# Kernel optimization log

Measured on AMD Instinct MI355X. Metric: run time of the kernel, lower is better.

## Reference

```python
import jax, jax.numpy as jnp
import numpy as np
import math

B, S, H, D = 8, 2048, 1024, 64  # batch, seq_len, hidden_dim, head_size

def setup_inputs() -> dict:
    key = jax.random.key(0)
    ks = jax.random.split(key, 7)
    lim = 1.0 / math.sqrt(H)  # torch Linear default init bound
    return {
        "x":  jax.random.normal(ks[0], (B, S, H), dtype=jnp.float32),
        "Wq": jax.random.uniform(ks[1], (H, D), jnp.float32, -lim, lim),
        "bq": jax.random.uniform(ks[2], (D,),   jnp.float32, -lim, lim),
        "Wk": jax.random.uniform(ks[3], (H, D), jnp.float32, -lim, lim),
        "bk": jax.random.uniform(ks[4], (D,),   jnp.float32, -lim, lim),
        "Wv": jax.random.uniform(ks[5], (H, D), jnp.float32, -lim, lim),
        "bv": jax.random.uniform(ks[6], (D,),   jnp.float32, -lim, lim),
    }

def reference(x, Wq, bq, Wk, bk, Wv, bv):
    # x: [B, S, H]
    q = x @ Wq + bq          # [B, S, D]
    k = x @ Wk + bk          # [B, S, D]
    v = x @ Wv + bv          # [B, S, D]
    scores = jnp.einsum("bsd,btd->bst", q, k)       # [B, S, S]
    causal = jnp.tril(jnp.ones((S, S), dtype=bool))
    scores = jnp.where(causal, scores, -jnp.inf)
    # NOTE: original module (faithfully) applies softmax FIRST, then divides
    # by sqrt(hidden_dim) -- it does NOT scale logits before softmax.
    weight = jax.nn.softmax(scores, axis=-1) / jnp.sqrt(jnp.float32(x.shape[-1]))
    # dropout p=0.0 -> identity
    return jnp.einsum("bst,btd->bsd", weight, v)     # [B, S, D]
```

## Files before the change

kernel.cpp:

```cpp
#include <hip/hip_runtime.h>


typedef float     f32x4 __attribute__((ext_vector_type(4)));
typedef _Float16  f16x8 __attribute__((ext_vector_type(8)));
typedef _Float16  f16x4 __attribute__((ext_vector_type(4)));

#define L2E 1.44269504088896340736f

__global__ __launch_bounds__(256) void wt_prep(const float* __restrict__ Wq,
                                               const float* __restrict__ Wk,
                                               const float* __restrict__ Wv,
                                               _Float16* __restrict__ WtF) {
  const int w  = blockIdx.x >> 4;
  const int kt = blockIdx.x & 15;
  const float* src = (w == 0) ? Wq : (w == 1 ? Wk : Wv);
  __shared__ _Float16 ls[64][72];
  const int t = threadIdx.x;
  {
    int rr = t >> 4;
    int c4 = (t & 15) * 4;
    #pragma unroll
    for (int ri = 0; ri < 4; ++ri) {
      int k = rr + ri * 16;
      f32x4 f = *(const f32x4*)&src[(size_t)(kt * 64 + k) * 64 + c4];
      #pragma unroll
      for (int j = 0; j < 4; ++j) ls[k][c4 + j] = (_Float16)f[j];
    }
  }
  __syncthreads();
  const int lane = t & 63, l16 = lane & 15, quad = lane >> 4;
  #pragma unroll
  for (int h = 0; h < 2; ++h) {
    int fid     = h * 4 + (t >> 6);
    int kstep_l = fid >> 2;
    int ntl     = fid & 3;
    int nt      = w * 4 + ntl;
    int kstep   = kt * 2 + kstep_l;
    f16x8 o;
    #pragma unroll
    for (int j = 0; j < 8; ++j) o[j] = ls[kstep_l * 32 + quad * 8 + j][ntl * 16 + l16];
    *(f16x8*)&WtF[((size_t)(kstep * 12 + nt) * 64 + lane) * 8] = o;
  }
}

__global__ __launch_bounds__(768) void qkv_gemm(const float* __restrict__ x,
                                                const _Float16* __restrict__ WtF,
                                                const float* __restrict__ bq,
                                                const float* __restrict__ bk,
                                                const float* __restrict__ bv,
                                                _Float16* __restrict__ qo,
                                                _Float16* __restrict__ ko,
                                                _Float16* __restrict__ vt) {
  __shared__ _Float16 xs[32 * 1024];
  const int tid  = threadIdx.x;
  const int wave = tid >> 6, lane = tid & 63;
  const int l16  = lane & 15, quad = lane >> 4;
  const int mhalf = wave / 6;
  const int ngrp  = wave - mhalf * 6;
  const int m0    = blockIdx.x * 32;

  if (tid < 512) {
    int row   = tid >> 4;
    int cbase = (tid & 15) * 4;
    const float* xrow = x + (size_t)(m0 + row) * 1024;
    int key = row & 7;
    #pragma unroll
    for (int j = 0; j < 16; ++j) {
      int col = cbase + j * 64;
      f32x4 f = *(const f32x4*)&xrow[col];
      f16x4 hh;
      #pragma unroll
      for (int e = 0; e < 4; ++e) hh[e] = (_Float16)f[e];
      int g   = col >> 3;
      int sub = col & 7;
      *(f16x4*)&xs[(size_t)row * 1024 + (size_t)((g ^ key) << 3) + sub] = hh;
    }
  }
  __syncthreads();

  f32x4 acc0 = (f32x4){0.f,0.f,0.f,0.f};
  f32x4 acc1 = (f32x4){0.f,0.f,0.f,0.f};
  const int arow = mhalf * 16 + l16;
  const _Float16* abase = xs + (size_t)arow * 1024;
  const int akey = arow & 7;
  const _Float16* wbase = WtF + ((size_t)(ngrp * 2) * 64 + lane) * 8;

  #pragma unroll 4
  for (int kstep = 0; kstep < 32; ++kstep) {
    f16x8 a = *(const f16x8*)(abase + (((kstep * 4 + quad) ^ akey) << 3));
    const _Float16* wk = wbase + (size_t)kstep * (12 * 64 * 8);
    f16x8 b0 = *(const f16x8*)(wk);
    f16x8 b1 = *(const f16x8*)(wk + 512);
    acc0 = __builtin_amdgcn_mfma_f32_16x16x32_f16(a, b0, acc0, 0, 0, 0);
    acc1 = __builtin_amdgcn_mfma_f32_16x16x32_f16(a, b1, acc1, 0, 0, 0);
  }

  f32x4 accs[2] = {acc0, acc1};
  #pragma unroll
  for (int i = 0; i < 2; ++i) {
    int nt  = ngrp * 2 + i;
    int col = nt * 16 + l16;
    float bias = (nt < 4) ? bq[col] : (nt < 8) ? bk[col - 64] : bv[col - 128];
    #pragma unroll
    for (int r = 0; r < 4; ++r) {
      int m = m0 + mhalf * 16 + quad * 4 + r;
      _Float16 hv = (_Float16)(accs[i][r] + bias);
      if (nt < 4)      qo[(size_t)m * 64 + col] = hv;
      else if (nt < 8) ko[(size_t)m * 64 + (col - 64)] = hv;
      else {
        int b = m >> 11, s = m & 2047;
        vt[((size_t)b * 64 + (col - 128)) * 2048 + s] = hv;
      }
    }
  }
}

__global__ __launch_bounds__(256) void attn(const _Float16* __restrict__ q,
                                            const _Float16* __restrict__ k,
                                            const _Float16* __restrict__ vt,
                                            _Float16* __restrict__ po,
                                            float* __restrict__ pm,
                                            float* __restrict__ pl) {
  const int bid = 575 - blockIdx.x;
  const int b   = blockIdx.y;
  int g = 0;
  #pragma unroll
  for (int gg = 0; gg < 7; ++gg) if (bid >= 8 * (gg + 1) * (gg + 2)) g = gg + 1;
  const int r   = bid - 8 * g * (g + 1);
  const int qi  = r / (g + 1);
  const int qt  = 16 * g + qi;
  const int s   = r - qi * (g + 1);
  const int q0  = qt * 16, kvend = q0 + 16;

  const int tid  = threadIdx.x;
  const int wave = tid >> 6, lane = tid & 63;
  const int l16  = lane & 15, quad = lane >> 4;
  const int kv0  = s * 256 + wave * 64;

  __shared__ float ow[4][64][17];
  __shared__ float mw[4][16], lw[4][16];
  _Float16* Plw = (_Float16*)&ow[wave][0][0];

  float m = -1e30f, l = 0.f;
  f32x4 o[4];
  #pragma unroll
  for (int i = 0; i < 4; ++i) o[i] = (f32x4){0.f, 0.f, 0.f, 0.f};

  if (kv0 < kvend) {
    const _Float16* qb = q  + (size_t)b * 2048 * 64;
    const _Float16* kb = k  + (size_t)b * 2048 * 64;
    const _Float16* vb = vt + (size_t)b * 64 * 2048;
    f16x8 qf0 = *(const f16x8*)&qb[(q0 + l16) * 64 + quad * 8];
    f16x8 qf1 = *(const f16x8*)&qb[(q0 + l16) * 64 + 32 + quad * 8];

    f32x4 sc[4];
    #pragma unroll
    for (int t = 0; t < 4; ++t) {
      int kvc = kv0 + t * 16;
      if (kvc < kvend) {
        f16x8 kf0 = *(const f16x8*)&kb[(kvc + l16) * 64 + quad * 8];
        f16x8 kf1 = *(const f16x8*)&kb[(kvc + l16) * 64 + 32 + quad * 8];
        f32x4 c = (f32x4){0.f, 0.f, 0.f, 0.f};
        c = __builtin_amdgcn_mfma_f32_16x16x32_f16(kf0, qf0, c, 0, 0, 0);
        c = __builtin_amdgcn_mfma_f32_16x16x32_f16(kf1, qf1, c, 0, 0, 0);
        sc[t] = c;
      } else sc[t] = (f32x4){-1e30f, -1e30f, -1e30f, -1e30f};
    }
    if (kv0 + 63 > q0) {
      #pragma unroll
      for (int t = 0; t < 4; ++t) {
        #pragma unroll
        for (int rr = 0; rr < 4; ++rr) {
          int skv = kv0 + t * 16 + quad * 4 + rr;
          if (skv > q0 + l16) sc[t][rr] = -1e30f;
        }
      }
    }
    float mx = sc[0][0];
    #pragma unroll
    for (int t = 0; t < 4; ++t)
      #pragma unroll
      for (int rr = 0; rr < 4; ++rr) mx = fmaxf(mx, sc[t][rr]);
    mx = fmaxf(mx, __shfl_xor(mx, 16, 64));
    mx = fmaxf(mx, __shfl_xor(mx, 32, 64));
    m = mx;
    float sum = 0.f;
    #pragma unroll
    for (int t = 0; t < 4; ++t)
      #pragma unroll
      for (int rr = 0; rr < 4; ++rr) {
        float e = exp2f((sc[t][rr] - m) * L2E);
        sc[t][rr] = e;
        sum += e;
      }
    sum += __shfl_xor(sum, 16, 64);
    sum += __shfl_xor(sum, 32, 64);
    l = sum;
    #pragma unroll
    for (int t = 0; t < 4; ++t)
      #pragma unroll
      for (int rr = 0; rr < 4; ++rr)
        Plw[l16 * 72 + t * 16 + quad * 4 + rr] = (_Float16)sc[t][rr];
    asm volatile("s_waitcnt lgkmcnt(0)" ::: "memory");
    f16x8 p0 = *(const f16x8*)&Plw[l16 * 72 + quad * 8];
    f16x8 p1 = *(const f16x8*)&Plw[l16 * 72 + 32 + quad * 8];
    #pragma unroll
    for (int dt = 0; dt < 4; ++dt) {
      f16x8 v0 = *(const f16x8*)&vb[(size_t)(dt * 16 + l16) * 2048 + kv0 + quad * 8];
      f16x8 v1 = *(const f16x8*)&vb[(size_t)(dt * 16 + l16) * 2048 + kv0 + 32 + quad * 8];
      o[dt] = __builtin_amdgcn_mfma_f32_16x16x32_f16(v0, p0, o[dt], 0, 0, 0);
      o[dt] = __builtin_amdgcn_mfma_f32_16x16x32_f16(v1, p1, o[dt], 0, 0, 0);
    }
  }

  __syncthreads();
  #pragma unroll
  for (int dt = 0; dt < 4; ++dt)
    #pragma unroll
    for (int rr = 0; rr < 4; ++rr)
      ow[wave][dt * 16 + quad * 4 + rr][l16] = o[dt][rr];
  if (quad == 0) { mw[wave][l16] = m; lw[wave][l16] = l; }
  __syncthreads();

  {
    int qrow = tid >> 4, d4 = (tid & 15) * 4;
    float m0v = mw[0][qrow], m1v = mw[1][qrow], m2v = mw[2][qrow], m3v = mw[3][qrow];
    float M = fmaxf(fmaxf(m0v, m1v), fmaxf(m2v, m3v));
    float w0 = exp2f((m0v - M) * L2E), w1 = exp2f((m1v - M) * L2E);
    float w2 = exp2f((m2v - M) * L2E), w3 = exp2f((m3v - M) * L2E);
    float L = w0 * lw[0][qrow] + w1 * lw[1][qrow] + w2 * lw[2][qrow] + w3 * lw[3][qrow];
    size_t pid = (size_t)b * 576 + bid;
    f16x4 oh;
    #pragma unroll
    for (int j = 0; j < 4; ++j)
      oh[j] = (_Float16)(w0 * ow[0][d4 + j][qrow] + w1 * ow[1][d4 + j][qrow]
                       + w2 * ow[2][d4 + j][qrow] + w3 * ow[3][d4 + j][qrow]);
    *(f16x4*)&po[pid * 1024 + (size_t)qrow * 64 + d4] = oh;
    if ((tid & 15) == 0) { pm[pid * 16 + qrow] = M; pl[pid * 16 + qrow] = L; }
  }
}

__global__ __launch_bounds__(256) void attn_merge(const _Float16* __restrict__ po,
                                                  const float* __restrict__ pm,
                                                  const float* __restrict__ pl,
                                                  float* __restrict__ out) {
  const int qt = blockIdx.x, b = blockIdx.y;
  const int g = qt >> 4, S = g + 1;
  const size_t base = (size_t)b * 576 + (size_t)(g + 1) * (8 * g + (qt & 15));
  const int t = threadIdx.x, qrow = t >> 4, d4 = (t & 15) * 4;

  float M = -1e30f;
  for (int s = 0; s < S; ++s) M = fmaxf(M, pm[(base + s) * 16 + qrow]);
  float L = 0.f;
  float O0 = 0.f, O1 = 0.f, O2 = 0.f, O3 = 0.f;
  for (int s = 0; s < S; ++s) {
    float w = exp2f((pm[(base + s) * 16 + qrow] - M) * L2E);
    L += w * pl[(base + s) * 16 + qrow];
    f16x4 ov = *(const f16x4*)&po[(base + s) * 1024 + (size_t)qrow * 64 + d4];
    O0 += w * (float)ov[0]; O1 += w * (float)ov[1];
    O2 += w * (float)ov[2]; O3 += w * (float)ov[3];
  }
  float inv = 1.0f / (L * 32.0f);
  f32x4 res = (f32x4){O0 * inv, O1 * inv, O2 * inv, O3 * inv};
  *(f32x4*)&out[((size_t)b * 2048 + qt * 16 + qrow) * 64 + d4] = res;
}

extern "C" void kernel_launch(void* const* d_in, const int* in_sizes, int n_in,
                              void* d_out, int out_size, void* d_ws, size_t ws_size,
                              hipStream_t stream) {
  const float* x  = (const float*)d_in[0];
  const float* Wq = (const float*)d_in[1];
  const float* bq = (const float*)d_in[2];
  const float* Wk = (const float*)d_in[3];
  const float* bk = (const float*)d_in[4];
  const float* Wv = (const float*)d_in[5];
  const float* bv = (const float*)d_in[6];
  float* out = (float*)d_out;

  _Float16* WtF = (_Float16*)d_ws;
  _Float16* qo  = WtF + 192 * 1024;
  _Float16* ko  = qo + 16384 * 64;
  _Float16* vt  = ko + 16384 * 64;
  _Float16* po  = vt + 8 * 64 * 2048;
  float*    pm  = (float*)(po + (size_t)4608 * 1024);
  float*    pl  = pm + 4608 * 16;

  hipLaunchKernelGGL(wt_prep,    dim3(48),       dim3(256), 0, stream, Wq, Wk, Wv, WtF);
  hipLaunchKernelGGL(qkv_gemm,   dim3(512),      dim3(768), 0, stream, x, WtF, bq, bk, bv, qo, ko, vt);
  hipLaunchKernelGGL(attn,       dim3(576, 8),   dim3(256), 0, stream, qo, ko, vt, po, pm, pl);
  hipLaunchKernelGGL(attn_merge, dim3(128, 8),   dim3(256), 0, stream, po, pm, pl, out);
}
```

Before: 162.9 us.

## Coarsen attention work split, write short rows directly, shrink QKV block

The attention kernel now gives each wave 256 KV positions instead of 64, and uses at most two KV splits per query tile instead of up to eight. Query tiles below 64 write the final normalized output directly, and only the upper tiles go through a simpler two-way merge. This cuts partial-result traffic and merge work. Separately, the QKV GEMM uses 512-thread blocks where each wave computes three N tiles instead of two. In exchange there are fewer attention blocks (192x8 instead of 576x8), more register pressure from sixteen score tiles per wave, and less parallelism overall.

Result: slower. 172.3 us (+5.8%).

```diff
diff --git a/kernel.cpp b/kernel.cpp
--- a/kernel.cpp
+++ b/kernel.cpp
@@ -43,23 +43,23 @@
   }
 }
 
-__global__ __launch_bounds__(768) void qkv_gemm(const float* __restrict__ x,
-                                                const _Float16* __restrict__ WtF,
-                                                const float* __restrict__ bq,
-                                                const float* __restrict__ bk,
-                                                const float* __restrict__ bv,
-                                                _Float16* __restrict__ qo,
-                                                _Float16* __restrict__ ko,
-                                                _Float16* __restrict__ vt) {
+__global__ __launch_bounds__(512, 4) void qkv_gemm(const float* __restrict__ x,
+                                                   const _Float16* __restrict__ WtF,
+                                                   const float* __restrict__ bq,
+                                                   const float* __restrict__ bk,
+                                                   const float* __restrict__ bv,
+                                                   _Float16* __restrict__ qo,
+                                                   _Float16* __restrict__ ko,
+                                                   _Float16* __restrict__ vt) {
   __shared__ _Float16 xs[32 * 1024];
   const int tid  = threadIdx.x;
   const int wave = tid >> 6, lane = tid & 63;
   const int l16  = lane & 15, quad = lane >> 4;
-  const int mhalf = wave / 6;
-  const int ngrp  = wave - mhalf * 6;
+  const int mhalf = wave >> 2;
+  const int ngrp  = wave & 3;
   const int m0    = blockIdx.x * 32;
 
-  if (tid < 512) {
+  {
     int row   = tid >> 4;
     int cbase = (tid & 15) * 4;
     const float* xrow = x + (size_t)(m0 + row) * 1024;
@@ -80,25 +80,28 @@
 
   f32x4 acc0 = (f32x4){0.f,0.f,0.f,0.f};
   f32x4 acc1 = (f32x4){0.f,0.f,0.f,0.f};
+  f32x4 acc2 = (f32x4){0.f,0.f,0.f,0.f};
   const int arow = mhalf * 16 + l16;
   const _Float16* abase = xs + (size_t)arow * 1024;
   const int akey = arow & 7;
-  const _Float16* wbase = WtF + ((size_t)(ngrp * 2) * 64 + lane) * 8;
-
-  #pragma unroll 4
+  const _Float16* wbase = WtF + ((size_t)(ngrp * 3) * 64 + lane) * 8;
+
+  #pragma unroll 8
   for (int kstep = 0; kstep < 32; ++kstep) {
     f16x8 a = *(const f16x8*)(abase + (((kstep * 4 + quad) ^ akey) << 3));
     const _Float16* wk = wbase + (size_t)kstep * (12 * 64 * 8);
     f16x8 b0 = *(const f16x8*)(wk);
     f16x8 b1 = *(const f16x8*)(wk + 512);
+    f16x8 b2 = *(const f16x8*)(wk + 1024);
     acc0 = __builtin_amdgcn_mfma_f32_16x16x32_f16(a, b0, acc0, 0, 0, 0);
     acc1 = __builtin_amdgcn_mfma_f32_16x16x32_f16(a, b1, acc1, 0, 0, 0);
-  }
-
-  f32x4 accs[2] = {acc0, acc1};
-  #pragma unroll
-  for (int i = 0; i < 2; ++i) {
-    int nt  = ngrp * 2 + i;
+    acc2 = __builtin_amdgcn_mfma_f32_16x16x32_f16(a, b2, acc2, 0, 0, 0);
+  }
+
+  f32x4 accs[3] = {acc0, acc1, acc2};
+  #pragma unroll
+  for (int i = 0; i < 3; ++i) {
+    int nt  = ngrp * 3 + i;
     int col = nt * 16 + l16;
     float bias = (nt < 4) ? bq[col] : (nt < 8) ? bk[col - 64] : bv[col - 128];
     #pragma unroll
@@ -115,70 +118,63 @@
   }
 }
 
-__global__ __launch_bounds__(256) void attn(const _Float16* __restrict__ q,
-                                            const _Float16* __restrict__ k,
-                                            const _Float16* __restrict__ vt,
-                                            _Float16* __restrict__ po,
-                                            float* __restrict__ pm,
-                                            float* __restrict__ pl) {
-  const int bid = 575 - blockIdx.x;
-  const int b   = blockIdx.y;
-  int g = 0;
-  #pragma unroll
-  for (int gg = 0; gg < 7; ++gg) if (bid >= 8 * (gg + 1) * (gg + 2)) g = gg + 1;
-  const int r   = bid - 8 * g * (g + 1);
-  const int qi  = r / (g + 1);
-  const int qt  = 16 * g + qi;
-  const int s   = r - qi * (g + 1);
-  const int q0  = qt * 16, kvend = q0 + 16;
-
+__global__ __launch_bounds__(256, 3) void attn(const _Float16* __restrict__ q,
+                                               const _Float16* __restrict__ k,
+                                               const _Float16* __restrict__ vt,
+                                               _Float16* __restrict__ po,
+                                               float* __restrict__ pm,
+                                               float* __restrict__ pl,
+                                               float* __restrict__ out) {
+  const int bx = blockIdx.x, b = blockIdx.y;
+  int qt, s;
+  if (bx < 128) { qt = 64 + (bx >> 1); s = bx & 1; }
+  else          { qt = 191 - bx;       s = 0; }
+  const int q0 = qt * 16, kvend = q0 + 16;
   const int tid  = threadIdx.x;
   const int wave = tid >> 6, lane = tid & 63;
   const int l16  = lane & 15, quad = lane >> 4;
-  const int kv0  = s * 256 + wave * 64;
-
-  __shared__ float ow[4][64][17];
+  const int kv0  = s * 1024 + wave * 256;
+  const int vlen = kvend - kv0;
+
+  __shared__ _Float16 Pbuf[4][16 * 264];
   __shared__ float mw[4][16], lw[4][16];
-  _Float16* Plw = (_Float16*)&ow[wave][0][0];
+  _Float16* Pw = &Pbuf[wave][0];
 
   float m = -1e30f, l = 0.f;
   f32x4 o[4];
   #pragma unroll
   for (int i = 0; i < 4; ++i) o[i] = (f32x4){0.f, 0.f, 0.f, 0.f};
 
-  if (kv0 < kvend) {
+  if (vlen > 0) {
     const _Float16* qb = q  + (size_t)b * 2048 * 64;
     const _Float16* kb = k  + (size_t)b * 2048 * 64;
     const _Float16* vb = vt + (size_t)b * 64 * 2048;
-    f16x8 qf0 = *(const f16x8*)&qb[(q0 + l16) * 64 + quad * 8];
-    f16x8 qf1 = *(const f16x8*)&qb[(q0 + l16) * 64 + 32 + quad * 8];
-
-    f32x4 sc[4];
-    #pragma unroll
-    for (int t = 0; t < 4; ++t) {
-      int kvc = kv0 + t * 16;
-      if (kvc < kvend) {
-        f16x8 kf0 = *(const f16x8*)&kb[(kvc + l16) * 64 + quad * 8];
-        f16x8 kf1 = *(const f16x8*)&kb[(kvc + l16) * 64 + 32 + quad * 8];
+    f16x8 qf0 = *(const f16x8*)&qb[(size_t)(q0 + l16) * 64 + quad * 8];
+    f16x8 qf1 = *(const f16x8*)&qb[(size_t)(q0 + l16) * 64 + 32 + quad * 8];
+
+    f32x4 sc[16];
+    #pragma unroll
+    for (int t = 0; t < 16; ++t) {
+      const int kvt = kv0 + t * 16;
+      if (kvt < kvend) {
+        f16x8 kf0 = *(const f16x8*)&kb[(size_t)(kvt + l16) * 64 + quad * 8];
+        f16x8 kf1 = *(const f16x8*)&kb[(size_t)(kvt + l16) * 64 + 32 + quad * 8];
         f32x4 c = (f32x4){0.f, 0.f, 0.f, 0.f};
         c = __builtin_amdgcn_mfma_f32_16x16x32_f16(kf0, qf0, c, 0, 0, 0);
         c = __builtin_amdgcn_mfma_f32_16x16x32_f16(kf1, qf1, c, 0, 0, 0);
+        if (kvt == q0) {
+          #pragma unroll
+          for (int rr = 0; rr < 4; ++rr)
+            if (quad * 4 + rr > l16) c[rr] = -1e30f;
+        }
         sc[t] = c;
-      } else sc[t] = (f32x4){-1e30f, -1e30f, -1e30f, -1e30f};
-    }
-    if (kv0 + 63 > q0) {
-      #pragma unroll
-      for (int t = 0; t < 4; ++t) {
-        #pragma unroll
-        for (int rr = 0; rr < 4; ++rr) {
-          int skv = kv0 + t * 16 + quad * 4 + rr;
-          if (skv > q0 + l16) sc[t][rr] = -1e30f;
-        }
+      } else {
+        sc[t] = (f32x4){-1e30f, -1e30f, -1e30f, -1e30f};
       }
     }
     float mx = sc[0][0];
     #pragma unroll
-    for (int t = 0; t < 4; ++t)
+    for (int t = 0; t < 16; ++t)
       #pragma unroll
       for (int rr = 0; rr < 4; ++rr) mx = fmaxf(mx, sc[t][rr]);
     mx = fmaxf(mx, __shfl_xor(mx, 16, 64));
@@ -186,57 +182,75 @@
     m = mx;
     float sum = 0.f;
     #pragma unroll
-    for (int t = 0; t < 4; ++t)
+    for (int t = 0; t < 16; ++t) {
       #pragma unroll
       for (int rr = 0; rr < 4; ++rr) {
         float e = exp2f((sc[t][rr] - m) * L2E);
         sc[t][rr] = e;
         sum += e;
       }
+    }
     sum += __shfl_xor(sum, 16, 64);
     sum += __shfl_xor(sum, 32, 64);
     l = sum;
     #pragma unroll
-    for (int t = 0; t < 4; ++t)
-      #pragma unroll
-      for (int rr = 0; rr < 4; ++rr)
-        Plw[l16 * 72 + t * 16 + quad * 4 + rr] = (_Float16)sc[t][rr];
+    for (int t = 0; t < 16; ++t) {
+      f16x4 ph;
+      #pragma unroll
+      for (int rr = 0; rr < 4; ++rr) ph[rr] = (_Float16)sc[t][rr];
+      *(f16x4*)&Pw[l16 * 264 + t * 16 + quad * 4] = ph;
+    }
     asm volatile("s_waitcnt lgkmcnt(0)" ::: "memory");
-    f16x8 p0 = *(const f16x8*)&Plw[l16 * 72 + quad * 8];
-    f16x8 p1 = *(const f16x8*)&Plw[l16 * 72 + 32 + quad * 8];
-    #pragma unroll
-    for (int dt = 0; dt < 4; ++dt) {
-      f16x8 v0 = *(const f16x8*)&vb[(size_t)(dt * 16 + l16) * 2048 + kv0 + quad * 8];
-      f16x8 v1 = *(const f16x8*)&vb[(size_t)(dt * 16 + l16) * 2048 + kv0 + 32 + quad * 8];
-      o[dt] = __builtin_amdgcn_mfma_f32_16x16x32_f16(v0, p0, o[dt], 0, 0, 0);
-      o[dt] = __builtin_amdgcn_mfma_f32_16x16x32_f16(v1, p1, o[dt], 0, 0, 0);
-    }
-  }
-
-  __syncthreads();
+    const int nck = (vlen >= 256) ? 8 : ((vlen + 31) >> 5);
+    #pragma unroll
+    for (int c = 0; c < 8; ++c) {
+      if (c < nck) {
+        f16x8 pfr = *(const f16x8*)&Pw[l16 * 264 + c * 32 + quad * 8];
+        #pragma unroll
+        for (int dt = 0; dt < 4; ++dt) {
+          f16x8 vf = *(const f16x8*)&vb[(size_t)(dt * 16 + l16) * 2048 + kv0 + c * 32 + quad * 8];
+          o[dt] = __builtin_amdgcn_mfma_f32_16x16x32_f16(vf, pfr, o[dt], 0, 0, 0);
+        }
+      }
+    }
+  }
+
+  float* owp = (float*)Pw;
   #pragma unroll
   for (int dt = 0; dt < 4; ++dt)
-    #pragma unroll
-    for (int rr = 0; rr < 4; ++rr)
-      ow[wave][dt * 16 + quad * 4 + rr][l16] = o[dt][rr];
+    *(f32x4*)&owp[l16 * 68 + dt * 16 + quad * 4] = o[dt];
   if (quad == 0) { mw[wave][l16] = m; lw[wave][l16] = l; }
   __syncthreads();
 
   {
-    int qrow = tid >> 4, d4 = (tid & 15) * 4;
-    float m0v = mw[0][qrow], m1v = mw[1][qrow], m2v = mw[2][qrow], m3v = mw[3][qrow];
+    const int qr = tid >> 4, dg = (tid & 15) * 4;
+    float m0v = mw[0][qr], m1v = mw[1][qr], m2v = mw[2][qr], m3v = mw[3][qr];
     float M = fmaxf(fmaxf(m0v, m1v), fmaxf(m2v, m3v));
-    float w0 = exp2f((m0v - M) * L2E), w1 = exp2f((m1v - M) * L2E);
-    float w2 = exp2f((m2v - M) * L2E), w3 = exp2f((m3v - M) * L2E);
-    float L = w0 * lw[0][qrow] + w1 * lw[1][qrow] + w2 * lw[2][qrow] + w3 * lw[3][qrow];
-    size_t pid = (size_t)b * 576 + bid;
-    f16x4 oh;
-    #pragma unroll
-    for (int j = 0; j < 4; ++j)
-      oh[j] = (_Float16)(w0 * ow[0][d4 + j][qrow] + w1 * ow[1][d4 + j][qrow]
-                       + w2 * ow[2][d4 + j][qrow] + w3 * ow[3][d4 + j][qrow]);
-    *(f16x4*)&po[pid * 1024 + (size_t)qrow * 64 + d4] = oh;
-    if ((tid & 15) == 0) { pm[pid * 16 + qrow] = M; pl[pid * 16 + qrow] = L; }
+    float L = 0.f;
+    f32x4 O = (f32x4){0.f, 0.f, 0.f, 0.f};
+    #pragma unroll
+    for (int w = 0; w < 4; ++w) {
+      float mwv = (w == 0) ? m0v : (w == 1) ? m1v : (w == 2) ? m2v : m3v;
+      float wt = exp2f((mwv - M) * L2E);
+      L += wt * lw[w][qr];
+      f32x4 ov = *(const f32x4*)&((float*)&Pbuf[w][0])[qr * 68 + dg];
+      #pragma unroll
+      for (int j = 0; j < 4; ++j) O[j] += wt * ov[j];
+    }
+    if (qt < 64) {
+      float inv = 1.0f / (L * 32.0f);
+      f32x4 res;
+      #pragma unroll
+      for (int j = 0; j < 4; ++j) res[j] = O[j] * inv;
+      *(f32x4*)&out[((size_t)b * 2048 + q0 + qr) * 64 + dg] = res;
+    } else {
+      size_t pid = (size_t)b * 128 + bx;
+      f16x4 oh;
+      #pragma unroll
+      for (int j = 0; j < 4; ++j) oh[j] = (_Float16)O[j];
+      *(f16x4*)&po[pid * 1024 + (size_t)qr * 64 + dg] = oh;
+      if ((tid & 15) == 0) { pm[pid * 16 + qr] = M; pl[pid * 16 + qr] = L; }
+    }
   }
 }
 
@@ -244,25 +258,22 @@
                                                   const float* __restrict__ pm,
                                                   const float* __restrict__ pl,
                                                   float* __restrict__ out) {
-  const int qt = blockIdx.x, b = blockIdx.y;
-  const int g = qt >> 4, S = g + 1;
-  const size_t base = (size_t)b * 576 + (size_t)(g + 1) * (8 * g + (qt & 15));
-  const int t = threadIdx.x, qrow = t >> 4, d4 = (t & 15) * 4;
-
-  float M = -1e30f;
-  for (int s = 0; s < S; ++s) M = fmaxf(M, pm[(base + s) * 16 + qrow]);
-  float L = 0.f;
-  float O0 = 0.f, O1 = 0.f, O2 = 0.f, O3 = 0.f;
-  for (int s = 0; s < S; ++s) {
-    float w = exp2f((pm[(base + s) * 16 + qrow] - M) * L2E);
-    L += w * pl[(base + s) * 16 + qrow];
-    f16x4 ov = *(const f16x4*)&po[(base + s) * 1024 + (size_t)qrow * 64 + d4];
-    O0 += w * (float)ov[0]; O1 += w * (float)ov[1];
-    O2 += w * (float)ov[2]; O3 += w * (float)ov[3];
-  }
+  const int qt = 64 + blockIdx.x, b = blockIdx.y;
+  const size_t pid0 = (size_t)b * 128 + (qt - 64) * 2, pid1 = pid0 + 1;
+  const int t = threadIdx.x, qr = t >> 4, dg = (t & 15) * 4;
+
+  float m0 = pm[pid0 * 16 + qr], m1 = pm[pid1 * 16 + qr];
+  float M  = fmaxf(m0, m1);
+  float w0 = exp2f((m0 - M) * L2E), w1 = exp2f((m1 - M) * L2E);
+  float L  = w0 * pl[pid0 * 16 + qr] + w1 * pl[pid1 * 16 + qr];
+  f16x4 o0 = *(const f16x4*)&po[pid0 * 1024 + (size_t)qr * 64 + dg];
+  f16x4 o1 = *(const f16x4*)&po[pid1 * 1024 + (size_t)qr * 64 + dg];
   float inv = 1.0f / (L * 32.0f);
-  f32x4 res = (f32x4){O0 * inv, O1 * inv, O2 * inv, O3 * inv};
-  *(f32x4*)&out[((size_t)b * 2048 + qt * 16 + qrow) * 64 + d4] = res;
+  f32x4 res;
+  #pragma unroll
+  for (int j = 0; j < 4; ++j)
+    res[j] = (w0 * (float)o0[j] + w1 * (float)o1[j]) * inv;
+  *(f32x4*)&out[((size_t)b * 2048 + qt * 16 + qr) * 64 + dg] = res;
 }
 
 extern "C" void kernel_launch(void* const* d_in, const int* in_sizes, int n_in,
@@ -282,11 +293,11 @@
   _Float16* ko  = qo + 16384 * 64;
   _Float16* vt  = ko + 16384 * 64;
   _Float16* po  = vt + 8 * 64 * 2048;
-  float*    pm  = (float*)(po + (size_t)4608 * 1024);
-  float*    pl  = pm + 4608 * 16;
-
-  hipLaunchKernelGGL(wt_prep,    dim3(48),       dim3(256), 0, stream, Wq, Wk, Wv, WtF);
-  hipLaunchKernelGGL(qkv_gemm,   dim3(512),      dim3(768), 0, stream, x, WtF, bq, bk, bv, qo, ko, vt);
-  hipLaunchKernelGGL(attn,       dim3(576, 8),   dim3(256), 0, stream, qo, ko, vt, po, pm, pl);
-  hipLaunchKernelGGL(attn_merge, dim3(128, 8),   dim3(256), 0, stream, po, pm, pl, out);
-}
+  float*    pm  = (float*)(po + (size_t)1024 * 1024);
+  float*    pl  = pm + 1024 * 16;
+
+  hipLaunchKernelGGL(wt_prep,    dim3(48),      dim3(256), 0, stream, Wq, Wk, Wv, WtF);
+  hipLaunchKernelGGL(qkv_gemm,   dim3(512),     dim3(512), 0, stream, x, WtF, bq, bk, bv, qo, ko, vt);
+  hipLaunchKernelGGL(attn,       dim3(192, 8),  dim3(256), 0, stream, qo, ko, vt, po, pm, pl, out);
+  hipLaunchKernelGGL(attn_merge, dim3(64, 8),   dim3(256), 0, stream, po, pm, pl, out);
+}
```
